# Kernel optimization log

Hardware: AMD Instinct MI355X
Metric: run time of the kernel (lower is better)

Reference implementation:

```python
import jax, jax.numpy as jnp
import numpy as np

N_NODES = 100000
N_EDGES = 1600000
N_GRAPHS = 512


def _graph_conv(x, W, b, src, dst, n_nodes):
    """DGL GraphConv, norm='both': D_in^-1/2 (A (D_out^-1/2 x)) W + b.
    Weight is applied on the smaller-dim side (same math, less memory)."""
    ones = jnp.ones(src.shape[0], dtype=x.dtype)
    deg_out = jnp.clip(jax.ops.segment_sum(ones, src, num_segments=n_nodes), 1.0)
    deg_in = jnp.clip(jax.ops.segment_sum(ones, dst, num_segments=n_nodes), 1.0)
    h = x * (deg_out ** -0.5)[:, None]
    if W.shape[0] > W.shape[1]:  # reduce feature dim before the SpMM
        h = h @ W
        h = jax.ops.segment_sum(h[src], dst, num_segments=n_nodes)
    else:
        h = jax.ops.segment_sum(h[src], dst, num_segments=n_nodes)
        h = h @ W
    return h * (deg_in ** -0.5)[:, None] + b


def setup_inputs() -> dict:
    key = jax.random.key(0)
    ks = jax.random.split(key, 16)
    x = jax.random.normal(ks[0], (N_NODES, 128), dtype=jnp.float32)
    src = jax.random.randint(ks[1], (N_EDGES,), 0, N_NODES, dtype=jnp.int32)
    dst = jax.random.randint(ks[2], (N_EDGES,), 0, N_NODES, dtype=jnp.int32)
    graph_ids = jnp.sort(jax.random.randint(ks[3], (N_NODES,), 0, N_GRAPHS, dtype=jnp.int32))
    s = 0.05
    return {
        "x": x, "src": src, "dst": dst, "graph_ids": graph_ids,
        "W1": jax.random.normal(ks[4], (128, 256), jnp.float32) * s,
        "b1": jnp.zeros((256,), jnp.float32),
        "W2": jax.random.normal(ks[5], (256, 64), jnp.float32) * s,
        "b2": jnp.zeros((64,), jnp.float32),
        "Wc1": jax.random.normal(ks[6], (64, 18), jnp.float32) * s,
        "bc1": jnp.zeros((18,), jnp.float32),
        "Wc2": jax.random.normal(ks[7], (18, 12), jnp.float32) * s,
        "bc2": jnp.zeros((12,), jnp.float32),
        "Wc3": jax.random.normal(ks[8], (12, 6), jnp.float32) * s,
        "bc3": jnp.zeros((6,), jnp.float32),
        "Wc4": jax.random.normal(ks[9], (6, 2), jnp.float32) * s,
        "bc4": jnp.zeros((2,), jnp.float32),
    }


def reference(x, src, dst, graph_ids, W1, b1, W2, b2, Wc1, bc1, Wc2, bc2, Wc3, bc3, Wc4, bc4):
    n = x.shape[0]
    h = jax.nn.relu(_graph_conv(x, W1, b1, src, dst, n))
    h = jax.nn.relu(_graph_conv(h, W2, b2, src, dst, n))
    # dgl.mean_nodes: per-graph mean over nodes
    sums = jax.ops.segment_sum(h, graph_ids, num_segments=N_GRAPHS)
    cnts = jnp.clip(jax.ops.segment_sum(jnp.ones(n, h.dtype), graph_ids, num_segments=N_GRAPHS), 1.0)
    hg = sums / cnts[:, None]
    # classifier: 4 stacked Linear layers, no activations (faithful to source)
    hg = hg @ Wc1 + bc1
    hg = hg @ Wc2 + bc2
    hg = hg @ Wc3 + bc3
    return hg @ Wc4 + bc4
```

## Files before the change

kernel.cpp:

```cpp
#include <hip/hip_runtime.h>
#include <cstdint>
#include <cstddef>

#define NGRAPHS 512

static inline size_t align_up(size_t x, size_t a){ return (x + a - 1) & ~(a - 1); }

__device__ __forceinline__ unsigned short f2bf(float f){
  unsigned int u = __float_as_uint(f);
  u += 0x7FFFu + ((u >> 16) & 1u);
  return (unsigned short)(u >> 16);
}
__device__ __forceinline__ float bflo(unsigned int u){ return __uint_as_float(u << 16); }
__device__ __forceinline__ float bfhi(unsigned int u){ return __uint_as_float(u & 0xffff0000u); }
__device__ __forceinline__ unsigned int pack2(float a, float b){
  return (unsigned)f2bf(a) | ((unsigned)f2bf(b) << 16);
}

typedef __attribute__((ext_vector_type(8))) short bf16x8;
typedef __attribute__((ext_vector_type(4))) float f32x4;

__global__ __launch_bounds__(256) void k_partcount(const int* __restrict__ src, const int* __restrict__ dst,
                                                   int* __restrict__ cntS, int* __restrict__ cntD, int n_edges){
  __shared__ int cs[256], cd[256];
  int tid = threadIdx.x;
  cs[tid] = 0; cd[tid] = 0;
  __syncthreads();
  int e0 = blockIdx.x * 4096;
  int e1 = min(e0 + 4096, n_edges);
  for (int e = e0 + tid; e < e1; e += 256){
    atomicAdd(&cs[src[e] >> 9], 1);
    atomicAdd(&cd[dst[e] >> 9], 1);
  }
  __syncthreads();
  cntS[blockIdx.x * 256 + tid] = cs[tid];
  cntD[blockIdx.x * 256 + tid] = cd[tid];
}

__global__ __launch_bounds__(256) void k_colscan(int* __restrict__ cntS, int* __restrict__ cntD,
                                                 int* __restrict__ totS, int* __restrict__ totD,
                                                 int nblk, int NB){
  int col = blockIdx.x;
  int* cnt; int* tot; int k;
  if (col < NB){ cnt = cntS; tot = totS; k = col; }
  else         { cnt = cntD; tot = totD; k = col - NB; }
  __shared__ int tsum[256];
  int tid = threadIdx.x;
  int i0 = 2 * tid, i1 = 2 * tid + 1;
  int a = (i0 < nblk) ? cnt[i0 * 256 + k] : 0;
  int b = (i1 < nblk) ? cnt[i1 * 256 + k] : 0;
  int s = a + b;
  tsum[tid] = s;
  __syncthreads();
  for (int off = 1; off < 256; off <<= 1){
    int t = (tid >= off) ? tsum[tid - off] : 0;
    __syncthreads();
    tsum[tid] += t;
    __syncthreads();
  }
  int pre = tsum[tid] - s;
  if (i0 < nblk) cnt[i0 * 256 + k] = pre;
  if (i1 < nblk) cnt[i1 * 256 + k] = pre + a;
  if (tid == 255) tot[k] = tsum[255];
}

__global__ __launch_bounds__(256) void k_scatter_det(const int* __restrict__ src, const int* __restrict__ dst,
                                                     const int* __restrict__ cntS, const int* __restrict__ cntD,
                                                     const int* __restrict__ totS, const int* __restrict__ totD,
                                                     int* __restrict__ baseS, int* __restrict__ baseD,
                                                     int2* __restrict__ pairD, int* __restrict__ srcS,
                                                     int n_edges, int NB){
  __shared__ int s1[256], s2[256], curS[256], curD[256];
  int tid = threadIdx.x;
  int b = blockIdx.x;
  int v1 = (tid < NB) ? totS[tid] : 0;
  int v2 = (tid < NB) ? totD[tid] : 0;
  s1[tid] = v1; s2[tid] = v2;
  __syncthreads();
  for (int off = 1; off < 256; off <<= 1){
    int t1 = (tid >= off) ? s1[tid - off] : 0;
    int t2 = (tid >= off) ? s2[tid - off] : 0;
    __syncthreads();
    s1[tid] += t1; s2[tid] += t2;
    __syncthreads();
  }
  int bS = s1[tid] - v1, bD = s2[tid] - v2;
  if (b == 0 && tid < NB){ baseS[tid] = bS; baseD[tid] = bD; }
  curS[tid] = bS + cntS[b * 256 + tid];
  curD[tid] = bD + cntD[b * 256 + tid];
  __syncthreads();
  int e0 = b * 4096, e1 = min(e0 + 4096, n_edges);
  for (int e = e0 + tid; e < e1; e += 256){
    int s = src[e], d = dst[e];
    int pd = atomicAdd(&curD[d >> 9], 1);
    pairD[pd] = make_int2(s, d);
    int ps = atomicAdd(&curS[s >> 9], 1);
    srcS[ps] = s;
  }
}

__global__ __launch_bounds__(256) void k_bucket_build(const int2* __restrict__ pairD, const int* __restrict__ baseD,
                                                      const int* __restrict__ srcS, const int* __restrict__ baseS,
                                                      int* __restrict__ offs, float* __restrict__ din_s,
                                                      float* __restrict__ dout_s, int* __restrict__ csr_src,
                                                      int NB, int n, int n_edges){
  __shared__ int cd[512], cs[512], cur[512];
  __shared__ int tsum[256];
  int b = blockIdx.x, node0 = b << 9, tid = threadIdx.x;
  int nn = min(512, n - node0);
  for (int i = tid; i < 512; i += 256){ cd[i] = 0; cs[i] = 0; }
  __syncthreads();
  int jd0 = baseD[b], jd1 = (b + 1 < NB) ? baseD[b + 1] : n_edges;
  for (int j = jd0 + tid; j < jd1; j += 256) atomicAdd(&cd[pairD[j].y - node0], 1);
  int js0 = baseS[b], js1 = (b + 1 < NB) ? baseS[b + 1] : n_edges;
  for (int j = js0 + tid; j < js1; j += 256) atomicAdd(&cs[srcS[j] - node0], 1);
  __syncthreads();
  int a0 = cd[2 * tid], a1 = cd[2 * tid + 1];
  int s = a0 + a1;
  tsum[tid] = s;
  __syncthreads();
  for (int off = 1; off < 256; off <<= 1){
    int t = (tid >= off) ? tsum[tid - off] : 0;
    __syncthreads();
    tsum[tid] += t;
    __syncthreads();
  }
  int pre = tsum[tid] - s + jd0;
  cur[2 * tid]     = pre;
  cur[2 * tid + 1] = pre + a0;
  __syncthreads();
  for (int i = tid; i < nn; i += 256){
    offs[node0 + i]   = cur[i];
    din_s[node0 + i]  = 1.0f / sqrtf((float)max(cd[i], 1));
    dout_s[node0 + i] = 1.0f / sqrtf((float)max(cs[i], 1));
  }
  if (b == NB - 1 && tid == 0) offs[n] = n_edges;
  __syncthreads();
  for (int j = jd0 + tid; j < jd1; j += 256){
    int2 e = pairD[j];
    int p = atomicAdd(&cur[e.y - node0], 1);
    csr_src[p] = e.x;
  }
}

__global__ __launch_bounds__(256) void k_prep(const float* __restrict__ x, unsigned int* __restrict__ xb,
                                              long long total4,
                                              const float* __restrict__ W1, unsigned short* __restrict__ Wt1,
                                              const float* __restrict__ W2, unsigned short* __restrict__ Wt2,
                                              float* __restrict__ sums, int* __restrict__ cnts){
  long long t = (long long)blockIdx.x * 256 + threadIdx.x;
  if (t < total4){
    float4 v = ((const float4*)x)[t];
    xb[t * 2 + 0] = pack2(v.x, v.y);
    xb[t * 2 + 1] = pack2(v.z, v.w);
    return;
  }
  long long u = t - total4;
  if (u < 128 * 256){
    int k = (int)(u / 256), n = (int)(u % 256);
    Wt1[(size_t)n * 128 + k] = f2bf(W1[u]);
    return;
  }
  u -= 128 * 256;
  if (u < 256 * 64){
    int k = (int)(u / 64), n = (int)(u % 64);
    Wt2[(size_t)n * 256 + k] = f2bf(W2[u]);
    return;
  }
  u -= 256 * 64;
  if (u < (long long)NGRAPHS * 64){ sums[u] = 0.f; return; }
  u -= (long long)NGRAPHS * 64;
  if (u < NGRAPHS) cnts[u] = 0;
}

__global__ __launch_bounds__(256) void k_spmm1(const unsigned int* __restrict__ xb,
    const int* __restrict__ offs, const int* __restrict__ csr_src,
    const float* __restrict__ dout_s, unsigned int* __restrict__ aggb, int n_nodes){
  int node = (blockIdx.x * blockDim.x + threadIdx.x) >> 5;
  int lane = threadIdx.x & 31;
  if (node >= n_nodes) return;
  int j0 = offs[node], j1 = offs[node + 1];
  const uint2* xp = (const uint2*)xb;
  float4 acc = make_float4(0.f, 0.f, 0.f, 0.f);
  int j = j0;
  for (; j + 4 <= j1; j += 4){
    int s0 = csr_src[j + 0];
    int s1 = csr_src[j + 1];
    int s2 = csr_src[j + 2];
    int s3 = csr_src[j + 3];
    float c0 = dout_s[s0];
    float c1 = dout_s[s1];
    float c2 = dout_s[s2];
    float c3 = dout_s[s3];
    uint2 v0 = xp[(size_t)s0 * 32 + lane];
    uint2 v1 = xp[(size_t)s1 * 32 + lane];
    uint2 v2 = xp[(size_t)s2 * 32 + lane];
    uint2 v3 = xp[(size_t)s3 * 32 + lane];
    acc.x = fmaf(bflo(v0.x), c0, acc.x); acc.y = fmaf(bfhi(v0.x), c0, acc.y);
    acc.z = fmaf(bflo(v0.y), c0, acc.z); acc.w = fmaf(bfhi(v0.y), c0, acc.w);
    acc.x = fmaf(bflo(v1.x), c1, acc.x); acc.y = fmaf(bfhi(v1.x), c1, acc.y);
    acc.z = fmaf(bflo(v1.y), c1, acc.z); acc.w = fmaf(bfhi(v1.y), c1, acc.w);
    acc.x = fmaf(bflo(v2.x), c2, acc.x); acc.y = fmaf(bfhi(v2.x), c2, acc.y);
    acc.z = fmaf(bflo(v2.y), c2, acc.z); acc.w = fmaf(bfhi(v2.y), c2, acc.w);
    acc.x = fmaf(bflo(v3.x), c3, acc.x); acc.y = fmaf(bfhi(v3.x), c3, acc.y);
    acc.z = fmaf(bflo(v3.y), c3, acc.z); acc.w = fmaf(bfhi(v3.y), c3, acc.w);
  }
  for (; j < j1; ++j){
    int s = csr_src[j];
    float sc = dout_s[s];
    uint2 v = xp[(size_t)s * 32 + lane];
    acc.x = fmaf(bflo(v.x), sc, acc.x); acc.y = fmaf(bfhi(v.x), sc, acc.y);
    acc.z = fmaf(bflo(v.y), sc, acc.z); acc.w = fmaf(bfhi(v.y), sc, acc.w);
  }
  uint2 pk;
  pk.x = pack2(acc.x, acc.y);
  pk.y = pack2(acc.z, acc.w);
  ((uint2*)aggb)[(size_t)node * 32 + lane] = pk;
}

__global__ __launch_bounds__(256) void k_spmm2(const unsigned short* __restrict__ t2,
    const int* __restrict__ offs, const int* __restrict__ csr_src,
    const float* __restrict__ din_s, const float* __restrict__ b2,
    float* __restrict__ h2, int n_nodes){
  int node = (blockIdx.x * blockDim.x + threadIdx.x) >> 5;
  int lane = threadIdx.x & 31;
  if (node >= n_nodes) return;
  int j0 = offs[node], j1 = offs[node + 1];
  const unsigned int* tp = (const unsigned int*)t2;
  float ax = 0.f, ay = 0.f;
  int j = j0;
  for (; j + 4 <= j1; j += 4){
    int s0 = csr_src[j + 0];
    int s1 = csr_src[j + 1];
    int s2 = csr_src[j + 2];
    int s3 = csr_src[j + 3];
    unsigned int v0 = tp[(size_t)s0 * 32 + lane];
    unsigned int v1 = tp[(size_t)s1 * 32 + lane];
    unsigned int v2 = tp[(size_t)s2 * 32 + lane];
    unsigned int v3 = tp[(size_t)s3 * 32 + lane];
    ax += bflo(v0) + bflo(v1) + bflo(v2) + bflo(v3);
    ay += bfhi(v0) + bfhi(v1) + bfhi(v2) + bfhi(v3);
  }
  for (; j < j1; ++j){
    unsigned int v = tp[(size_t)csr_src[j] * 32 + lane];
    ax += bflo(v);
    ay += bfhi(v);
  }
  float ds = din_s[node];
  float2 bb = ((const float2*)b2)[lane];
  float2 r;
  r.x = fmaxf(fmaf(ax, ds, bb.x), 0.f);
  r.y = fmaxf(fmaf(ay, ds, bb.y), 0.f);
  ((float2*)h2)[(size_t)node * 32 + lane] = r;
}

template<bool C_BF16, bool EPI, bool EPI2>
__global__ __launch_bounds__(256) void gemm_mfma(
    const unsigned short* __restrict__ A, const unsigned short* __restrict__ Bt, void* __restrict__ Cp,
    int M, int N, int K,
    const float* __restrict__ rowScaleC, const float* __restrict__ rowScaleC2,
    const float* __restrict__ bias){
  constexpr int BM = 128, BN = 64, BK = 32, LDA = 40;
  __shared__ __align__(16) unsigned short As[2][BM * LDA];
  __shared__ __align__(16) unsigned short Bs[2][BN * LDA];
  int tid = threadIdx.x;
  int bm0 = blockIdx.x * BM;
  int bn0 = blockIdx.y * BN;
  int wid = tid >> 6, lane = tid & 63;
  int wm = (wid >> 1) * 64, wn = (wid & 1) * 32;
  int quad = lane >> 4, l16 = lane & 15;
  f32x4 acc[4][2];
#pragma unroll
  for (int t = 0; t < 4; ++t)
#pragma unroll
    for (int u = 0; u < 2; ++u) acc[t][u] = f32x4{0.f, 0.f, 0.f, 0.f};

  uint2 ar[4], br[2];
  auto preload = [&](int kk){
#pragma unroll
    for (int it = 0; it < 4; ++it){
      int i = tid + it * 256;
      int m = i >> 3, c = i & 7;
      int gr = bm0 + m;
      ar[it] = (gr < M) ? *(const uint2*)(A + (size_t)gr * K + kk + c * 4) : make_uint2(0u, 0u);
    }
#pragma unroll
    for (int it = 0; it < 2; ++it){
      int i = tid + it * 256;
      int n = i >> 3, c = i & 7;
      br[it] = *(const uint2*)(Bt + (size_t)(bn0 + n) * K + kk + c * 4);
    }
  };
  auto commit = [&](int buf){
#pragma unroll
    for (int it = 0; it < 4; ++it){
      int i = tid + it * 256;
      int m = i >> 3, c = i & 7;
      *(uint2*)&As[buf][m * LDA + c * 4] = ar[it];
    }
#pragma unroll
    for (int it = 0; it < 2; ++it){
      int i = tid + it * 256;
      int n = i >> 3, c = i & 7;
      *(uint2*)&Bs[buf][n * LDA + c * 4] = br[it];
    }
  };

  preload(0);
  commit(0);
  __syncthreads();
  int nk = K / BK;
  for (int kb = 0; kb < nk; ++kb){
    int cur = kb & 1;
    if (kb + 1 < nk) preload((kb + 1) * BK);
    bf16x8 af[4], bfr[2];
#pragma unroll
    for (int t = 0; t < 4; ++t)
      af[t] = *(const bf16x8*)&As[cur][(wm + t * 16 + l16) * LDA + quad * 8];
#pragma unroll
    for (int u = 0; u < 2; ++u)
      bfr[u] = *(const bf16x8*)&Bs[cur][(wn + u * 16 + l16) * LDA + quad * 8];
#pragma unroll
    for (int t = 0; t < 4; ++t)
#pragma unroll
      for (int u = 0; u < 2; ++u)
        acc[t][u] = __builtin_amdgcn_mfma_f32_16x16x32_bf16(af[t], bfr[u], acc[t][u], 0, 0, 0);
    if (kb + 1 < nk){
      commit(cur ^ 1);
      __syncthreads();
    }
  }
  float bv[2] = {0.f, 0.f};
  if constexpr (EPI){ bv[0] = bias[bn0 + wn + l16]; bv[1] = bias[bn0 + wn + 16 + l16]; }
#pragma unroll
  for (int t = 0; t < 4; ++t){
#pragma unroll
    for (int r = 0; r < 4; ++r){
      int gr = bm0 + wm + t * 16 + quad * 4 + r;
      if (gr < M){
        float rs = 1.f, rs2 = 1.f;
        if constexpr (EPI)  rs  = rowScaleC[gr];
        if constexpr (EPI2) rs2 = rowScaleC2[gr];
#pragma unroll
        for (int u = 0; u < 2; ++u){
          int gc = bn0 + wn + u * 16 + l16;
          float cv = acc[t][u][r];
          if constexpr (EPI)  cv = fmaxf(fmaf(cv, rs, bv[u]), 0.f);
          if constexpr (EPI2) cv *= rs2;
          if constexpr (C_BF16) ((unsigned short*)Cp)[(size_t)gr * N + gc] = f2bf(cv);
          else                  ((float*)Cp)[(size_t)gr * N + gc] = cv;
        }
      }
    }
  }
}

__global__ __launch_bounds__(256) void k_pool(const float* __restrict__ h2, const int* __restrict__ gids,
                                              float* __restrict__ sums, int* __restrict__ cnts, int n_nodes){
  int wave = (blockIdx.x * blockDim.x + threadIdx.x) >> 6;
  int lane = threadIdx.x & 63;
  int base = wave * 64;
  if (base >= n_nodes) return;
  int endn = min(base + 64, n_nodes);
  float acc = 0.f;
  int cur = -1, len = 0;
  for (int i = base; i < endn; ++i){
    int g = gids[i];
    float v = h2[(size_t)i * 64 + lane];
    if (g != cur){
      if (cur >= 0){
        atomicAdd(&sums[(size_t)cur * 64 + lane], acc);
        if (lane == 0) atomicAdd(&cnts[cur], len);
      }
      cur = g; acc = 0.f; len = 0;
    }
    acc += v; len++;
  }
  atomicAdd(&sums[(size_t)cur * 64 + lane], acc);
  if (lane == 0) atomicAdd(&cnts[cur], len);
}

__global__ __launch_bounds__(256) void k_classifier(const float* __restrict__ sums, const int* __restrict__ cnts,
    const float* __restrict__ Wc1, const float* __restrict__ bc1,
    const float* __restrict__ Wc2, const float* __restrict__ bc2,
    const float* __restrict__ Wc3, const float* __restrict__ bc3,
    const float* __restrict__ Wc4, const float* __restrict__ bc4,
    float* __restrict__ out){
  __shared__ float w1[64 * 18], w2[18 * 12], w3[12 * 6], w4[6 * 2];
  __shared__ float B1[18], B2[12], B3[6], B4[2];
  int tid = threadIdx.x;
  for (int i = tid; i < 64 * 18; i += 256) w1[i] = Wc1[i];
  for (int i = tid; i < 18 * 12; i += 256) w2[i] = Wc2[i];
  for (int i = tid; i < 12 * 6;  i += 256) w3[i] = Wc3[i];
  for (int i = tid; i < 6 * 2;   i += 256) w4[i] = Wc4[i];
  if (tid < 18) B1[tid] = bc1[tid];
  if (tid < 12) B2[tid] = bc2[tid];
  if (tid < 6)  B3[tid] = bc3[tid];
  if (tid < 2)  B4[tid] = bc4[tid];
  __syncthreads();
  int g = blockIdx.x * 256 + tid;
  float cnt = fmaxf((float)cnts[g], 1.0f);
  float h[64];
#pragma unroll
  for (int f = 0; f < 64; ++f) h[f] = sums[(size_t)g * 64 + f] / cnt;
  float t1[18];
#pragma unroll
  for (int j = 0; j < 18; ++j){
    float s = B1[j];
    for (int f = 0; f < 64; ++f) s = fmaf(h[f], w1[f * 18 + j], s);
    t1[j] = s;
  }
  float t2[12];
#pragma unroll
  for (int j = 0; j < 12; ++j){
    float s = B2[j];
    for (int f = 0; f < 18; ++f) s = fmaf(t1[f], w2[f * 12 + j], s);
    t2[j] = s;
  }
  float t3[6];
#pragma unroll
  for (int j = 0; j < 6; ++j){
    float s = B3[j];
    for (int f = 0; f < 12; ++f) s = fmaf(t2[f], w3[f * 6 + j], s);
    t3[j] = s;
  }
#pragma unroll
  for (int j = 0; j < 2; ++j){
    float s = B4[j];
    for (int f = 0; f < 6; ++f) s = fmaf(t3[f], w4[f * 2 + j], s);
    out[(size_t)g * 2 + j] = s;
  }
}

extern "C" void kernel_launch(void* const* d_in, const int* in_sizes, int n_in,
                              void* d_out, int out_size, void* d_ws, size_t ws_size,
                              hipStream_t stream){
  const float* x   = (const float*)d_in[0];
  const int*   src = (const int*)d_in[1];
  const int*   dst = (const int*)d_in[2];
  const int*   gid = (const int*)d_in[3];
  const float* W1  = (const float*)d_in[4];
  const float* b1  = (const float*)d_in[5];
  const float* W2  = (const float*)d_in[6];
  const float* b2  = (const float*)d_in[7];
  const float* Wc1 = (const float*)d_in[8];
  const float* bc1 = (const float*)d_in[9];
  const float* Wc2 = (const float*)d_in[10];
  const float* bc2 = (const float*)d_in[11];
  const float* Wc3 = (const float*)d_in[12];
  const float* bc3 = (const float*)d_in[13];
  const float* Wc4 = (const float*)d_in[14];
  const float* bc4 = (const float*)d_in[15];
  float* out = (float*)d_out;

  const int n_nodes = in_sizes[3];
  const int n_edges = in_sizes[1];
  const int F1 = 256, F2 = 64;
  const int NB   = (n_nodes + 511) >> 9;
  const int NBLK = (n_edges + 4095) / 4096;

  char* w = (char*)d_ws;
  size_t o = 0;
  auto alloc = [&](size_t bytes) -> char* {
    char* p = w + o;
    o = align_up(o + bytes, 256);
    return p;
  };
  float* sums      = (float*)alloc((size_t)NGRAPHS * F2 * 4);
  int*   cnts      = (int*)  alloc((size_t)NGRAPHS * 4);
  int*   cntS      = (int*)  alloc((size_t)NBLK * 256 * 4);
  int*   cntD      = (int*)  alloc((size_t)NBLK * 256 * 4);
  int*   totS      = (int*)  alloc((size_t)256 * 4);
  int*   totD      = (int*)  alloc((size_t)256 * 4);
  int*   baseS     = (int*)  alloc((size_t)256 * 4);
  int*   baseD     = (int*)  alloc((size_t)256 * 4);
  float* dout_s    = (float*)alloc((size_t)n_nodes * 4);
  float* din_s     = (float*)alloc((size_t)n_nodes * 4);
  int*   offs      = (int*)  alloc((size_t)(n_nodes + 1) * 4);
  int*   csr_src   = (int*)  alloc((size_t)n_edges * 4);
  unsigned short* Wt1 = (unsigned short*)alloc((size_t)256 * 128 * 2);
  unsigned short* Wt2 = (unsigned short*)alloc((size_t)64 * 256 * 2);
  unsigned int*   xb  = (unsigned int*)  alloc((size_t)n_nodes * 128 * 2);
  unsigned short* aggb= (unsigned short*)alloc((size_t)n_nodes * 128 * 2);
  unsigned short* h1b = (unsigned short*)alloc((size_t)n_nodes * F1 * 2);
  int2*  pairD = (int2*)aggb;
  int*   srcS  = (int*)((char*)aggb + (size_t)n_edges * 8);
  unsigned short* t2b = aggb;
  float* h2    = (float*)h1b;

  {
    long long total4 = (long long)n_nodes * 32;
    long long totalP = total4 + 128 * 256 + 256 * 64 + (long long)NGRAPHS * 64 + NGRAPHS;
    k_prep<<<(int)((totalP + 255) / 256), 256, 0, stream>>>(x, xb, total4, W1, Wt1, W2, Wt2, sums, cnts);
  }

  k_partcount   <<<NBLK, 256, 0, stream>>>(src, dst, cntS, cntD, n_edges);
  k_colscan     <<<2 * NB, 256, 0, stream>>>(cntS, cntD, totS, totD, NBLK, NB);
  k_scatter_det <<<NBLK, 256, 0, stream>>>(src, dst, cntS, cntD, totS, totD, baseS, baseD, pairD, srcS, n_edges, NB);
  k_bucket_build<<<NB, 256, 0, stream>>>(pairD, baseD, srcS, baseS, offs, din_s, dout_s, csr_src, NB, n_nodes, n_edges);

  int gx = (n_nodes + 127) / 128;
  {
    long long threads = (long long)n_nodes * 32;
    k_spmm1<<<(int)((threads + 255) / 256), 256, 0, stream>>>(xb, offs, csr_src, dout_s, (unsigned int*)aggb, n_nodes);
    gemm_mfma<true, true, true><<<dim3(gx, F1 / 64), 256, 0, stream>>>(
        aggb, Wt1, h1b, n_nodes, F1, 128, din_s, dout_s, b1);
  }
  {
    gemm_mfma<true, false, false><<<dim3(gx, 1), 256, 0, stream>>>(
        h1b, Wt2, t2b, n_nodes, F2, F1, nullptr, nullptr, nullptr);
    long long threads = (long long)n_nodes * 32;
    k_spmm2<<<(int)((threads + 255) / 256), 256, 0, stream>>>(t2b, offs, csr_src, din_s, b2, h2, n_nodes);
  }
  {
    int pool_waves = (n_nodes + 63) / 64;
    long long threads = (long long)pool_waves * 64;
    k_pool<<<(int)((threads + 255) / 256), 256, 0, stream>>>(h2, gid, sums, cnts, n_nodes);
    k_classifier<<<NGRAPHS / 256, 256, 0, stream>>>(sums, cnts, Wc1, bc1, Wc2, bc2, Wc3, bc3, Wc4, bc4, out);
  }
}
```

Baseline: 381.0 us.

## Fuse second SpMM with mean pooling using per-graph node boundaries

The second aggregation now writes straight into per-graph pooled sums instead of materialising the h2 feature matrix and running a separate pooling pass. Blocks are assigned by graph and chunk, each half-wave walks that graph's nodes, and partial sums are reduced in shared memory before a global atomic add. Graph node boundaries are built in the prep kernel from the sorted graph ids, and they also supply the per-graph counts, so the count atomics go away. This removes the h2 round trip and one launch. In exchange, only 2048 blocks run, with load set by graph size, so occupancy and balance may be worse than the per-node launch.

```diff
diff --git a/kernel.cpp b/kernel.cpp
--- a/kernel.cpp
+++ b/kernel.cpp
@@ -147,7 +147,8 @@
                                               long long total4,
                                               const float* __restrict__ W1, unsigned short* __restrict__ Wt1,
                                               const float* __restrict__ W2, unsigned short* __restrict__ Wt2,
-                                              float* __restrict__ sums, int* __restrict__ cnts){
+                                              float* __restrict__ sums,
+                                              const int* __restrict__ gids, int* __restrict__ gb, int n_nodes){
   long long t = (long long)blockIdx.x * 256 + threadIdx.x;
   if (t < total4){
     float4 v = ((const float4*)x)[t];
@@ -170,7 +171,14 @@
   u -= 256 * 64;
   if (u < (long long)NGRAPHS * 64){ sums[u] = 0.f; return; }
   u -= (long long)NGRAPHS * 64;
-  if (u < NGRAPHS) cnts[u] = 0;
+  if (u < n_nodes){
+    int i = (int)u;
+    int g  = gids[i];
+    int gp = (i > 0) ? gids[i - 1] : -1;
+    for (int q = gp + 1; q <= g; ++q) gb[q] = i;
+    if (i == n_nodes - 1)
+      for (int q = g + 1; q <= NGRAPHS; ++q) gb[q] = n_nodes;
+  }
 }
 
 __global__ __launch_bounds__(256) void k_spmm1(const unsigned int* __restrict__ xb,
@@ -218,40 +226,52 @@
   ((uint2*)aggb)[(size_t)node * 32 + lane] = pk;
 }
 
-__global__ __launch_bounds__(256) void k_spmm2(const unsigned short* __restrict__ t2,
+#define SCHUNK 4
+__global__ __launch_bounds__(256) void k_spmm2_fused(const unsigned short* __restrict__ t2,
     const int* __restrict__ offs, const int* __restrict__ csr_src,
     const float* __restrict__ din_s, const float* __restrict__ b2,
-    float* __restrict__ h2, int n_nodes){
-  int node = (blockIdx.x * blockDim.x + threadIdx.x) >> 5;
-  int lane = threadIdx.x & 31;
-  if (node >= n_nodes) return;
-  int j0 = offs[node], j1 = offs[node + 1];
+    const int* __restrict__ gb, float* __restrict__ sums){
+  __shared__ float bs[64];
+  int tid = threadIdx.x;
+  int g = blockIdx.x & (NGRAPHS - 1);
+  int chunk = blockIdx.x >> 9;
+  int hw = chunk * 8 + (tid >> 5);
+  int lane = tid & 31;
+  if (tid < 64) bs[tid] = 0.f;
+  __syncthreads();
+  int g0 = gb[g], g1 = gb[g + 1];
   const unsigned int* tp = (const unsigned int*)t2;
-  float ax = 0.f, ay = 0.f;
-  int j = j0;
-  for (; j + 4 <= j1; j += 4){
-    int s0 = csr_src[j + 0];
-    int s1 = csr_src[j + 1];
-    int s2 = csr_src[j + 2];
-    int s3 = csr_src[j + 3];
-    unsigned int v0 = tp[(size_t)s0 * 32 + lane];
-    unsigned int v1 = tp[(size_t)s1 * 32 + lane];
-    unsigned int v2 = tp[(size_t)s2 * 32 + lane];
-    unsigned int v3 = tp[(size_t)s3 * 32 + lane];
-    ax += bflo(v0) + bflo(v1) + bflo(v2) + bflo(v3);
-    ay += bfhi(v0) + bfhi(v1) + bfhi(v2) + bfhi(v3);
-  }
-  for (; j < j1; ++j){
-    unsigned int v = tp[(size_t)csr_src[j] * 32 + lane];
-    ax += bflo(v);
-    ay += bfhi(v);
-  }
-  float ds = din_s[node];
   float2 bb = ((const float2*)b2)[lane];
-  float2 r;
-  r.x = fmaxf(fmaf(ax, ds, bb.x), 0.f);
-  r.y = fmaxf(fmaf(ay, ds, bb.y), 0.f);
-  ((float2*)h2)[(size_t)node * 32 + lane] = r;
+  float sx = 0.f, sy = 0.f;
+  for (int node = g0 + hw; node < g1; node += 32){
+    int j0 = offs[node], j1 = offs[node + 1];
+    float ax = 0.f, ay = 0.f;
+    int j = j0;
+    for (; j + 4 <= j1; j += 4){
+      int s0 = csr_src[j + 0];
+      int s1 = csr_src[j + 1];
+      int s2 = csr_src[j + 2];
+      int s3 = csr_src[j + 3];
+      unsigned int v0 = tp[(size_t)s0 * 32 + lane];
+      unsigned int v1 = tp[(size_t)s1 * 32 + lane];
+      unsigned int v2 = tp[(size_t)s2 * 32 + lane];
+      unsigned int v3 = tp[(size_t)s3 * 32 + lane];
+      ax += bflo(v0) + bflo(v1) + bflo(v2) + bflo(v3);
+      ay += bfhi(v0) + bfhi(v1) + bfhi(v2) + bfhi(v3);
+    }
+    for (; j < j1; ++j){
+      unsigned int v = tp[(size_t)csr_src[j] * 32 + lane];
+      ax += bflo(v);
+      ay += bfhi(v);
+    }
+    float ds = din_s[node];
+    sx += fmaxf(fmaf(ax, ds, bb.x), 0.f);
+    sy += fmaxf(fmaf(ay, ds, bb.y), 0.f);
+  }
+  atomicAdd(&bs[2 * lane], sx);
+  atomicAdd(&bs[2 * lane + 1], sy);
+  __syncthreads();
+  if (tid < 64) atomicAdd(&sums[(size_t)g * 64 + tid], bs[tid]);
 }
 
 template<bool C_BF16, bool EPI, bool EPI2>
@@ -355,32 +375,7 @@
   }
 }
 
-__global__ __launch_bounds__(256) void k_pool(const float* __restrict__ h2, const int* __restrict__ gids,
-                                              float* __restrict__ sums, int* __restrict__ cnts, int n_nodes){
-  int wave = (blockIdx.x * blockDim.x + threadIdx.x) >> 6;
-  int lane = threadIdx.x & 63;
-  int base = wave * 64;
-  if (base >= n_nodes) return;
-  int endn = min(base + 64, n_nodes);
-  float acc = 0.f;
-  int cur = -1, len = 0;
-  for (int i = base; i < endn; ++i){
-    int g = gids[i];
-    float v = h2[(size_t)i * 64 + lane];
-    if (g != cur){
-      if (cur >= 0){
-        atomicAdd(&sums[(size_t)cur * 64 + lane], acc);
-        if (lane == 0) atomicAdd(&cnts[cur], len);
-      }
-      cur = g; acc = 0.f; len = 0;
-    }
-    acc += v; len++;
-  }
-  atomicAdd(&sums[(size_t)cur * 64 + lane], acc);
-  if (lane == 0) atomicAdd(&cnts[cur], len);
-}
-
-__global__ __launch_bounds__(256) void k_classifier(const float* __restrict__ sums, const int* __restrict__ cnts,
+__global__ __launch_bounds__(256) void k_classifier(const float* __restrict__ sums, const int* __restrict__ gb,
     const float* __restrict__ Wc1, const float* __restrict__ bc1,
     const float* __restrict__ Wc2, const float* __restrict__ bc2,
     const float* __restrict__ Wc3, const float* __restrict__ bc3,
@@ -399,7 +394,7 @@
   if (tid < 2)  B4[tid] = bc4[tid];
   __syncthreads();
   int g = blockIdx.x * 256 + tid;
-  float cnt = fmaxf((float)cnts[g], 1.0f);
+  float cnt = fmaxf((float)(gb[g + 1] - gb[g]), 1.0f);
   float h[64];
 #pragma unroll
   for (int f = 0; f < 64; ++f) h[f] = sums[(size_t)g * 64 + f] / cnt;
@@ -467,7 +462,7 @@
     return p;
   };
   float* sums      = (float*)alloc((size_t)NGRAPHS * F2 * 4);
-  int*   cnts      = (int*)  alloc((size_t)NGRAPHS * 4);
+  int*   gb        = (int*)  alloc((size_t)(NGRAPHS + 1) * 4);
   int*   cntS      = (int*)  alloc((size_t)NBLK * 256 * 4);
   int*   cntD      = (int*)  alloc((size_t)NBLK * 256 * 4);
   int*   totS      = (int*)  alloc((size_t)256 * 4);
@@ -486,12 +481,12 @@
   int2*  pairD = (int2*)aggb;
   int*   srcS  = (int*)((char*)aggb + (size_t)n_edges * 8);
   unsigned short* t2b = aggb;
-  float* h2    = (float*)h1b;
 
   {
     long long total4 = (long long)n_nodes * 32;
-    long long totalP = total4 + 128 * 256 + 256 * 64 + (long long)NGRAPHS * 64 + NGRAPHS;
-    k_prep<<<(int)((totalP + 255) / 256), 256, 0, stream>>>(x, xb, total4, W1, Wt1, W2, Wt2, sums, cnts);
+    long long totalP = total4 + 128 * 256 + 256 * 64 + (long long)NGRAPHS * 64 + n_nodes;
+    k_prep<<<(int)((totalP + 255) / 256), 256, 0, stream>>>(x, xb, total4, W1, Wt1, W2, Wt2,
+                                                            sums, gid, gb, n_nodes);
   }
 
   k_partcount   <<<NBLK, 256, 0, stream>>>(src, dst, cntS, cntD, n_edges);
@@ -509,13 +504,7 @@
   {
     gemm_mfma<true, false, false><<<dim3(gx, 1), 256, 0, stream>>>(
         h1b, Wt2, t2b, n_nodes, F2, F1, nullptr, nullptr, nullptr);
-    long long threads = (long long)n_nodes * 32;
-    k_spmm2<<<(int)((threads + 255) / 256), 256, 0, stream>>>(t2b, offs, csr_src, din_s, b2, h2, n_nodes);
-  }
-  {
-    int pool_waves = (n_nodes + 63) / 64;
-    long long threads = (long long)pool_waves * 64;
-    k_pool<<<(int)((threads + 255) / 256), 256, 0, stream>>>(h2, gid, sums, cnts, n_nodes);
-    k_classifier<<<NGRAPHS / 256, 256, 0, stream>>>(sums, cnts, Wc1, bc1, Wc2, bc2, Wc3, bc3, Wc4, bc4, out);
-  }
-}
+    k_spmm2_fused<<<NGRAPHS * SCHUNK, 256, 0, stream>>>(t2b, offs, csr_src, din_s, b2, gb, sums);
+  }
+  k_classifier<<<NGRAPHS / 256, 256, 0, stream>>>(sums, gb, Wc1, bc1, Wc2, bc2, Wc3, bc3, Wc4, bc4, out);
+}
```

After: 363.6 us. 1.05x faster.
